# Kernel optimization log

Measured on AMD Instinct MI355X. Metric: run time of the kernel, lower is better.

## Reference

```python
import jax, jax.numpy as jnp
import numpy as np

B, N, NODE_DIM = 32, 512, 2
D, H, L, FF = 512, 8, 3, 2048
DK = D // H  # key/val dim per head = 64
EPS = 1e-5


def batch_norm(h, gamma, beta):
    # BatchNorm1d in training mode over flattened (batch*graph) dim, biased var
    flat = h.reshape(-1, h.shape[-1])
    mu = flat.mean(axis=0)
    var = flat.var(axis=0)
    out = (flat - mu) * jax.lax.rsqrt(var + EPS) * gamma + beta
    return out.reshape(h.shape)


def mha(h, Wq, Wk, Wv, Wo):
    # h: [B,N,D]; Wq/Wk/Wv: [H,D,DK]; Wo: [H,DK,D]
    Q = jnp.einsum('bnd,hdk->hbnk', h, Wq)
    K = jnp.einsum('bnd,hdk->hbnk', h, Wk)
    V = jnp.einsum('bnd,hdk->hbnk', h, Wv)
    scores = jnp.einsum('hbqk,hbnk->hbqn', Q, K) / jnp.sqrt(jnp.float32(DK))
    attn = jax.nn.softmax(scores, axis=-1)
    heads = jnp.einsum('hbqn,hbnk->hbqk', attn, V)
    return jnp.einsum('hbqk,hkd->bqd', heads, Wo)


def setup_inputs() -> dict:
    key = jax.random.key(0)
    ks = jax.random.split(key, 16)
    u = lambda k, shape, fan: jax.random.uniform(k, shape, jnp.float32, -1.0, 1.0) / np.sqrt(fan)
    return {
        'x': jax.random.normal(ks[0], (B, N, NODE_DIM), jnp.float32),
        'We': u(ks[1], (D, NODE_DIM), NODE_DIM),
        'be': u(ks[2], (D,), NODE_DIM),
        'Wq': u(ks[3], (L, H, D, DK), DK),
        'Wk': u(ks[4], (L, H, D, DK), DK),
        'Wv': u(ks[5], (L, H, D, DK), DK),
        'Wo': u(ks[6], (L, H, DK, D), D),
        'g1': jnp.ones((L, D), jnp.float32),
        'b1': jnp.zeros((L, D), jnp.float32),
        'W1': u(ks[7], (L, FF, D), D),
        'bb1': u(ks[8], (L, FF), D),
        'W2': u(ks[9], (L, D, FF), FF),
        'bb2': u(ks[10], (L, D), FF),
        'g2': jnp.ones((L, D), jnp.float32),
        'b2': jnp.zeros((L, D), jnp.float32),
    }


def reference(x, We, be, Wq, Wk, Wv, Wo, g1, b1, W1, bb1, W2, bb2, g2, b2):
    # init embed: Linear(node_dim -> D)
    h = jnp.einsum('bnc,dc->bnd', x, We) + be
    for i in range(L):
        h = batch_norm(h + mha(h, Wq[i], Wk[i], Wv[i], Wo[i]), g1[i], b1[i])
        ff = jax.nn.relu(jnp.einsum('bnd,fd->bnf', h, W1[i]) + bb1[i])
        ff = jnp.einsum('bnf,df->bnd', ff, W2[i]) + bb2[i]
        h = batch_norm(h + ff, g2[i], b2[i])
    return h, h.mean(axis=1)
```

## Files before the change

kernel.cpp:

```cpp
#include <hip/hip_runtime.h>
#include <hip/hip_bf16.h>

#define Bx 32
#define Nx 512
#define Dx 512
#define Hx 8
#define DKx 64
#define FFx 2048
#define TOK (Bx * Nx)
#define EPSx 1e-5f

typedef float  f32x4  __attribute__((ext_vector_type(4)));
typedef _Float16 hfrag8 __attribute__((ext_vector_type(8)));
typedef _Float16 h4     __attribute__((ext_vector_type(4)));

struct hf2 { _Float16 hi, lo; };
__device__ __forceinline__ hf2 split2h(float v) {
    _Float16 h = (_Float16)v;
    hf2 r; r.hi = h; r.lo = (_Float16)(v - (float)h);
    return r;
}

__device__ __forceinline__ void gl16(const void* g, void* l) {
    __builtin_amdgcn_global_load_lds(
        (const __attribute__((address_space(1))) unsigned int*)g,
        (__attribute__((address_space(3))) unsigned int*)l, 16, 0, 0);
}

__device__ __forceinline__ int swzoff(int row, int q) {
    int p = row >> 1;
    int sl = ((row & 1) << 2) | q;
    int s = sl ^ (p & 7);
    return p * 128 + s * 16;
}

__device__ __forceinline__ float ldsel(const void* p32, const void* p16, size_t i, int f32) {
    return f32 ? ((const float*)p32)[i]
               : __bfloat162float(((const __hip_bfloat16*)p16)[i]);
}

__global__ void detect_kernel(const void* __restrict__ x, int* __restrict__ flag)
{
    if (threadIdx.x == 0 && blockIdx.x == 0) {
        const unsigned short* u = (const unsigned short*)x;
        int hits = 0;
        for (int i = 0; i < 256; ++i) {
            int e = (u[i] >> 7) & 0xFF;
            if (e >= 0x86) ++hits;
        }
        *flag = (hits > 8) ? 1 : 0;
    }
}

__global__ __launch_bounds__(256) void cvt_kernel(
    const void* __restrict__ W, _Float16* __restrict__ o, const int* __restrict__ dtp)
{
    const int f32 = *dtp;
    size_t idx = (size_t)blockIdx.x * 256 + threadIdx.x;
    o[idx] = (_Float16)ldsel(W, W, idx, f32);
}

__global__ __launch_bounds__(256) void transpose_cvt_kernel(
    const void* __restrict__ W, _Float16* __restrict__ o,
    int R, int C, const int* __restrict__ dtp)
{
    const int f32 = *dtp;
    __shared__ float tile[64][65];
    const size_t mbase = (size_t)blockIdx.z * R * C;
    const int c0 = blockIdx.x * 64, r0 = blockIdx.y * 64;
    const int tc = threadIdx.x & 63, tg = threadIdx.x >> 6;
    #pragma unroll
    for (int i = 0; i < 16; ++i) {
        int r = tg * 16 + i;
        tile[r][tc] = ldsel(W, W, mbase + (size_t)(r0 + r) * C + c0 + tc, f32);
    }
    __syncthreads();
    #pragma unroll
    for (int i = 0; i < 16; ++i) {
        int cc = tg * 16 + i;
        o[mbase + (size_t)(c0 + cc) * R + r0 + tc] = (_Float16)tile[tc][cc];
    }
}

__global__ __launch_bounds__(256) void embed_kernel(
    const void* __restrict__ x, const void* __restrict__ We,
    const void* __restrict__ be, _Float16* __restrict__ hh, _Float16* __restrict__ hl,
    const int* __restrict__ dtp)
{
    const int f32 = *dtp;
    size_t idx = (size_t)blockIdx.x * 256 + threadIdx.x;
    int d = idx & (Dx - 1);
    size_t t = idx >> 9;
    float v = ldsel(x, x, t * 2, f32)     * ldsel(We, We, d * 2, f32) +
              ldsel(x, x, t * 2 + 1, f32) * ldsel(We, We, d * 2 + 1, f32) +
              ldsel(be, be, d, f32);
    hf2 s = split2h(v);
    hh[idx] = s.hi; hl[idx] = s.lo;
}

template <int NMF, int EPI, int OHF, int STATS>
__global__ __launch_bounds__(256, NMF == 2 ? 3 : 4) void gemm3(
    const _Float16* __restrict__ Ahg, const _Float16* __restrict__ Alg,
    const _Float16* __restrict__ Bg,
    const void* __restrict__ bias32, const void* __restrict__ bias16,
    const _Float16* __restrict__ residH, const _Float16* __restrict__ residL,
    void* __restrict__ outp, float* __restrict__ part,
    int M, int N, int K, const int* __restrict__ dtp)
{
    constexpr int PLANES = NMF + 1;
    constexpr int BUFB = PLANES * 8192;
    constexpr int BOFF = NMF * 8192;
    const int f32 = *dtp;
    __shared__ __align__(16) unsigned char lds[2][BUFB];

    const int tid = threadIdx.x;
    const int gx = gridDim.x;
    const int nwg = gx * gridDim.y;
    int flat = blockIdx.y * gx + blockIdx.x;
    flat = (flat & 7) * (nwg >> 3) + (flat >> 3);
    const int bm = (flat / gx) * 128;
    const int bn = (flat % gx) * 128;

    const int lane = tid & 63, wv = tid >> 6;
    const int quad = lane >> 4, lrow = lane & 15;
    const int wm = (wv & 1) * 64, wn = (wv >> 1) * 64;

    f32x4 acc[4][4] = {};

    const int s2 = (lane & 7) ^ (lane >> 3);
    const int rl = 2 * (lane >> 3) + (s2 >> 2);
    const int cl = (s2 & 3) * 8;

    const _Float16* wsrc;
    int wrb;
    bool doStage;
    if constexpr (NMF == 2) {
        doStage = (wv < 3);
        wsrc = (wv == 0) ? Ahg : (wv == 1) ? Alg : Bg;
        wrb  = (wv < 2) ? bm : bn;
    } else {
        doStage = (wv < 2);
        wsrc = (wv == 0) ? Ahg : Bg;
        wrb  = (wv == 0) ? bm : bn;
    }

    auto stage = [&](int buf, int k0) {
        if (doStage) {
            const _Float16* s = wsrc + (size_t)(wrb + rl) * K + k0 + cl;
            #pragma unroll
            for (int ch = 0; ch < 8; ++ch)
                gl16(s + (size_t)(ch * 16) * K, &lds[buf][wv * 8192 + ch * 1024]);
        }
    };

    int offA[4], offB[4];
    #pragma unroll
    for (int mt = 0; mt < 4; ++mt) offA[mt] = swzoff(wm + mt * 16 + lrow, quad);
    #pragma unroll
    for (int nt = 0; nt < 4; ++nt) offB[nt] = BOFF + swzoff(wn + nt * 16 + lrow, quad);

    stage(0, 0);
    if (32 < K) stage(1, 32);

    int cur = 0;
    for (int k0 = 0; k0 < K; k0 += 32) {
        if (k0 + 32 < K) asm volatile("s_waitcnt vmcnt(8)" ::: "memory");
        else             asm volatile("s_waitcnt vmcnt(0)" ::: "memory");
        __builtin_amdgcn_sched_barrier(0);
        __builtin_amdgcn_s_barrier();
        __builtin_amdgcn_sched_barrier(0);

        __builtin_amdgcn_s_setprio(1);
        const unsigned char* bp = lds[cur];
        hfrag8 ah[4], alo[4];
        #pragma unroll
        for (int mt = 0; mt < 4; ++mt) {
            ah[mt] = *(const hfrag8*)(bp + offA[mt]);
            if constexpr (NMF == 2) alo[mt] = *(const hfrag8*)(bp + offA[mt] + 8192);
        }
        #pragma unroll
        for (int nt = 0; nt < 4; ++nt) {
            hfrag8 b = *(const hfrag8*)(bp + offB[nt]);
            #pragma unroll
            for (int mt = 0; mt < 4; ++mt) {
                acc[mt][nt] = __builtin_amdgcn_mfma_f32_16x16x32_f16(ah[mt], b, acc[mt][nt], 0, 0, 0);
                if constexpr (NMF == 2)
                    acc[mt][nt] = __builtin_amdgcn_mfma_f32_16x16x32_f16(alo[mt], b, acc[mt][nt], 0, 0, 0);
            }
        }
        __builtin_amdgcn_s_setprio(0);

        __builtin_amdgcn_sched_barrier(0);
        asm volatile("s_waitcnt lgkmcnt(0)" ::: "memory");
        __builtin_amdgcn_s_barrier();
        __builtin_amdgcn_sched_barrier(0);

        if (k0 + 64 < K) stage(cur, k0 + 64);
        cur ^= 1;
    }

    #pragma unroll
    for (int nt = 0; nt < 4; ++nt) {
        const int n = bn + wn + nt * 16 + lrow;
        float cs = 0.f, cq = 0.f;
        #pragma unroll
        for (int mt = 0; mt < 4; ++mt)
            #pragma unroll
            for (int reg = 0; reg < 4; ++reg) {
                int m = bm + wm + mt * 16 + quad * 4 + reg;
                float v = acc[mt][nt][reg];
                if constexpr (EPI == 1) { v += ldsel(bias32, bias16, n, f32); v = fmaxf(v, 0.f); }
                if constexpr (EPI == 2) {
                    if (bias32) v += ldsel(bias32, bias16, n, f32);
                    size_t ridx = (size_t)m * N + n;
                    v += (float)residH[ridx] + (float)residL[ridx];
                }
                if constexpr (OHF) ((_Float16*)outp)[(size_t)m * N + n] = (_Float16)v;
                else               ((float*)outp)[(size_t)m * N + n] = v;
                if constexpr (STATS) { cs += v; cq += v * v; }
            }
        if constexpr (STATS) {
            cs += __shfl_xor(cs, 16); cs += __shfl_xor(cs, 32);
            cq += __shfl_xor(cq, 16); cq += __shfl_xor(cq, 32);
            if (quad == 0) {
                float* pb = part + (size_t)(bm >> 7) * 1024;
                atomicAdd(&pb[n], cs);
                atomicAdd(&pb[512 + n], cq);
            }
        }
    }
}

__global__ __launch_bounds__(256, 3) void qkv_mfma(
    const _Float16* __restrict__ Ahg, const _Float16* __restrict__ Alg,
    const _Float16* __restrict__ QT, const _Float16* __restrict__ KT,
    const _Float16* __restrict__ VT,
    _Float16* __restrict__ Qhg, _Float16* __restrict__ Qlg,
    _Float16* __restrict__ Khg, _Float16* __restrict__ Vo, int M, int K)
{
    __shared__ __align__(16) unsigned char lds[2][3 * 8192];

    const int tid = threadIdx.x;
    const int gx = gridDim.x;
    const int nwg = gx * gridDim.y;
    int flat = blockIdx.y * gx + blockIdx.x;
    flat = (flat & 7) * (nwg >> 3) + (flat >> 3);
    const int bm = (flat / gx) * 128;
    const int bn = (flat % gx) * 128;

    const int sel = bn >> 9;
    const int nloc = bn & 511;
    const _Float16* Bg = ((sel == 0) ? QT : (sel == 1) ? KT : VT) + (size_t)nloc * K;

    const int lane = tid & 63, wv = tid >> 6;
    const int quad = lane >> 4, lrow = lane & 15;
    const int wm = (wv & 1) * 64, wn = (wv >> 1) * 64;

    f32x4 acc[4][4] = {};

    const int s2 = (lane & 7) ^ (lane >> 3);
    const int rl = 2 * (lane >> 3) + (s2 >> 2);
    const int cl = (s2 & 3) * 8;

    const bool doStage = (wv < 3);
    const _Float16* wsrc = (wv == 0) ? Ahg : (wv == 1) ? Alg : Bg;
    const int wrb = (wv < 2) ? bm : 0;

    auto stage = [&](int buf, int k0) {
        if (doStage) {
            const _Float16* s = wsrc + (size_t)(wrb + rl) * K + k0 + cl;
            #pragma unroll
            for (int ch = 0; ch < 8; ++ch)
                gl16(s + (size_t)(ch * 16) * K, &lds[buf][wv * 8192 + ch * 1024]);
        }
    };

    int offA[4], offB[4];
    #pragma unroll
    for (int mt = 0; mt < 4; ++mt) offA[mt] = swzoff(wm + mt * 16 + lrow, quad);
    #pragma unroll
    for (int nt = 0; nt < 4; ++nt) offB[nt] = 16384 + swzoff(wn + nt * 16 + lrow, quad);

    stage(0, 0);
    if (32 < K) stage(1, 32);

    int cur = 0;
    for (int k0 = 0; k0 < K; k0 += 32) {
        if (k0 + 32 < K) asm volatile("s_waitcnt vmcnt(8)" ::: "memory");
        else             asm volatile("s_waitcnt vmcnt(0)" ::: "memory");
        __builtin_amdgcn_sched_barrier(0);
        __builtin_amdgcn_s_barrier();
        __builtin_amdgcn_sched_barrier(0);

        __builtin_amdgcn_s_setprio(1);
        const unsigned char* bp = lds[cur];
        hfrag8 ah[4], alo[4];
        #pragma unroll
        for (int mt = 0; mt < 4; ++mt) {
            ah[mt]  = *(const hfrag8*)(bp + offA[mt]);
            alo[mt] = *(const hfrag8*)(bp + offA[mt] + 8192);
        }
        #pragma unroll
        for (int nt = 0; nt < 4; ++nt) {
            hfrag8 b = *(const hfrag8*)(bp + offB[nt]);
            #pragma unroll
            for (int mt = 0; mt < 4; ++mt) {
                acc[mt][nt] = __builtin_amdgcn_mfma_f32_16x16x32_f16(ah[mt],  b, acc[mt][nt], 0, 0, 0);
                acc[mt][nt] = __builtin_amdgcn_mfma_f32_16x16x32_f16(alo[mt], b, acc[mt][nt], 0, 0, 0);
            }
        }
        __builtin_amdgcn_s_setprio(0);

        __builtin_amdgcn_sched_barrier(0);
        asm volatile("s_waitcnt lgkmcnt(0)" ::: "memory");
        __builtin_amdgcn_s_barrier();
        __builtin_amdgcn_sched_barrier(0);

        if (k0 + 64 < K) stage(cur, k0 + 64);
        cur ^= 1;
    }

    const int nb = M >> 9;
    #pragma unroll
    for (int mt = 0; mt < 4; ++mt)
        #pragma unroll
        for (int nt = 0; nt < 4; ++nt) {
            const int ncol = nloc + wn + nt * 16 + lrow;
            const int head = ncol >> 6, dk = ncol & 63;
            const int m0 = bm + wm + mt * 16 + quad * 4;
            const int b_ = m0 >> 9, q = m0 & 511;
            if (sel == 2) {
                h4 v;
                #pragma unroll
                for (int reg = 0; reg < 4; ++reg) v[reg] = (_Float16)acc[mt][nt][reg];
                *(h4*)&Vo[(((size_t)head * nb + b_) * DKx + dk) * Nx + q] = v;
            } else if (sel == 1) {
                #pragma unroll
                for (int reg = 0; reg < 4; ++reg) {
                    size_t oidx = (((size_t)head * nb + b_) * Nx + (q + reg)) * DKx + dk;
                    Khg[oidx] = (_Float16)acc[mt][nt][reg];
                }
            } else {
                #pragma unroll
                for (int reg = 0; reg < 4; ++reg) {
                    hf2 s = split2h(acc[mt][nt][reg]);
                    size_t oidx = (((size_t)head * nb + b_) * Nx + (q + reg)) * DKx + dk;
                    Qhg[oidx] = s.hi;
                    Qlg[oidx] = s.lo;
                }
            }
        }
}

__global__ __launch_bounds__(256, 4) void attn_kernel(
    const _Float16* __restrict__ Qhg, const _Float16* __restrict__ Qlg,
    const _Float16* __restrict__ Khg, const _Float16* __restrict__ Vtg,
    _Float16* __restrict__ headsH, _Float16* __restrict__ headsL)
{
    __shared__ __align__(16) _Float16  Kh[64][72];
    __shared__ __align__(16) _Float16  Vt[64][72];
    __shared__ __align__(16) _Float16  Sp[64][72];
    __shared__ float ml[64], ll[64], al[64];

    const int tid = threadIdx.x;
    const int q0 = blockIdx.x * 64;
    const int hb = blockIdx.y;
    const size_t base = (size_t)hb * (Nx * DKx);
    const int lane = tid & 63, wv = tid >> 6;
    const int quad = lane >> 4, lrow = lane & 15;
    const int wm = (wv & 1) * 32, wn = (wv >> 1) * 32;
    const int sr = tid >> 2, sc = (tid & 3) * 16;

    {
        size_t off = base + (size_t)(q0 + sr) * DKx + sc;
        *(hfrag8*)&Kh[sr][sc]     = *(const hfrag8*)(Qhg + off);
        *(hfrag8*)&Kh[sr][sc + 8] = *(const hfrag8*)(Qhg + off + 8);
        *(hfrag8*)&Sp[sr][sc]     = *(const hfrag8*)(Qlg + off);
        *(hfrag8*)&Sp[sr][sc + 8] = *(const hfrag8*)(Qlg + off + 8);
    }
    if (tid < 64) { ml[tid] = -INFINITY; ll[tid] = 0.f; }
    __syncthreads();

    hfrag8 qh[2][2], qlo[2][2];
    #pragma unroll
    for (int mt = 0; mt < 2; ++mt)
        #pragma unroll
        for (int ks = 0; ks < 2; ++ks) {
            qh[mt][ks]  = *(const hfrag8*)&Kh[wm + mt * 16 + lrow][ks * 32 + quad * 8];
            qlo[mt][ks] = *(const hfrag8*)&Sp[wm + mt * 16 + lrow][ks * 32 + quad * 8];
        }
    __syncthreads();

    hfrag8 pkh[2], pv[2];
    auto loadKV = [&](int n0) {
        size_t off = base + (size_t)(n0 + sr) * DKx + sc;
        pkh[0] = *(const hfrag8*)(Khg + off);
        pkh[1] = *(const hfrag8*)(Khg + off + 8);
        const _Float16* vp = Vtg + base + (size_t)sr * Nx + n0 + sc;
        pv[0] = *(const hfrag8*)vp;
        pv[1] = *(const hfrag8*)(vp + 8);
    };
    auto storeKV = [&]() {
        *(hfrag8*)&Kh[sr][sc]     = pkh[0];
        *(hfrag8*)&Kh[sr][sc + 8] = pkh[1];
        *(hfrag8*)&Vt[sr][sc]     = pv[0];
        *(hfrag8*)&Vt[sr][sc + 8] = pv[1];
    };

    f32x4 accO[2][2] = {};

    loadKV(0); storeKV();
    __syncthreads();

    for (int n0 = 0; n0 < Nx; n0 += 64) {
        const bool more = (n0 + 64 < Nx);
        if (more) loadKV(n0 + 64);

        f32x4 accS[2][2] = {};
        __builtin_amdgcn_s_setprio(1);
        #pragma unroll
        for (int ks = 0; ks < 2; ++ks) {
            hfrag8 bh[2];
            #pragma unroll
            for (int nt = 0; nt < 2; ++nt)
                bh[nt] = *(const hfrag8*)&Kh[wn + nt * 16 + lrow][ks * 32 + quad * 8];
            #pragma unroll
            for (int mt = 0; mt < 2; ++mt)
                #pragma unroll
                for (int nt = 0; nt < 2; ++nt) {
                    accS[mt][nt] = __builtin_amdgcn_mfma_f32_16x16x32_f16(qh[mt][ks],  bh[nt], accS[mt][nt], 0, 0, 0);
                    accS[mt][nt] = __builtin_amdgcn_mfma_f32_16x16x32_f16(qlo[mt][ks], bh[nt], accS[mt][nt], 0, 0, 0);
                }
        }
        __builtin_amdgcn_s_setprio(0);
        #pragma unroll
        for (int mt = 0; mt < 2; ++mt)
            #pragma unroll
            for (int nt = 0; nt < 2; ++nt)
                #pragma unroll
                for (int reg = 0; reg < 4; ++reg)
                    Sp[wm + mt * 16 + quad * 4 + reg][wn + nt * 16 + lrow] =
                        (_Float16)(accS[mt][nt][reg] * 0.125f);
        __syncthreads();

        {
            hfrag8 s0 = *(const hfrag8*)&Sp[sr][sc];
            hfrag8 s1 = *(const hfrag8*)&Sp[sr][sc + 8];
            float rmax = -INFINITY;
            #pragma unroll
            for (int j = 0; j < 8; ++j) {
                rmax = fmaxf(rmax, (float)s0[j]);
                rmax = fmaxf(rmax, (float)s1[j]);
            }
            rmax = fmaxf(rmax, __shfl_xor(rmax, 1));
            rmax = fmaxf(rmax, __shfl_xor(rmax, 2));
            float mold = ml[sr];
            float mnew = fmaxf(mold, rmax);
            float sum = 0.f;
            hfrag8 p0, p1;
            #pragma unroll
            for (int j = 0; j < 8; ++j) {
                float pa = __expf((float)s0[j] - mnew);
                float pb = __expf((float)s1[j] - mnew);
                sum += pa + pb;
                p0[j] = (_Float16)pa;
                p1[j] = (_Float16)pb;
            }
            sum += __shfl_xor(sum, 1);
            sum += __shfl_xor(sum, 2);
            *(hfrag8*)&Sp[sr][sc]     = p0;
            *(hfrag8*)&Sp[sr][sc + 8] = p1;
            if ((tid & 3) == 0) {
                float alpha = __expf(mold - mnew);
                ml[sr] = mnew;
                ll[sr] = ll[sr] * alpha + sum;
                al[sr] = alpha;
            }
        }
        __syncthreads();

        #pragma unroll
        for (int mt = 0; mt < 2; ++mt) {
            float a0 = al[wm + mt * 16 + quad * 4 + 0];
            float a1 = al[wm + mt * 16 + quad * 4 + 1];
            float a2 = al[wm + mt * 16 + quad * 4 + 2];
            float a3 = al[wm + mt * 16 + quad * 4 + 3];
            #pragma unroll
            for (int nt = 0; nt < 2; ++nt) {
                accO[mt][nt][0] *= a0; accO[mt][nt][1] *= a1;
                accO[mt][nt][2] *= a2; accO[mt][nt][3] *= a3;
            }
        }
        __builtin_amdgcn_s_setprio(1);
        #pragma unroll
        for (int ks = 0; ks < 2; ++ks) {
            hfrag8 ap[2], bv[2];
            #pragma unroll
            for (int mt = 0; mt < 2; ++mt)
                ap[mt] = *(const hfrag8*)&Sp[wm + mt * 16 + lrow][ks * 32 + quad * 8];
            #pragma unroll
            for (int nt = 0; nt < 2; ++nt)
                bv[nt] = *(const hfrag8*)&Vt[wn + nt * 16 + lrow][ks * 32 + quad * 8];
            #pragma unroll
            for (int mt = 0; mt < 2; ++mt)
                #pragma unroll
                for (int nt = 0; nt < 2; ++nt)
                    accO[mt][nt] = __builtin_amdgcn_mfma_f32_16x16x32_f16(ap[mt], bv[nt], accO[mt][nt], 0, 0, 0);
        }
        __builtin_amdgcn_s_setprio(0);

        if (more) {
            __syncthreads();
            storeKV();
            __syncthreads();
        }
    }

    const int h_ = hb >> 5, b_ = hb & 31;
    #pragma unroll
    for (int mt = 0; mt < 2; ++mt)
        #pragma unroll
        for (int reg = 0; reg < 4; ++reg) {
            int qrow = wm + mt * 16 + quad * 4 + reg;
            float invl = 1.f / ll[qrow];
            size_t tok = (size_t)b_ * Nx + (q0 + qrow);
            #pragma unroll
            for (int nt = 0; nt < 2; ++nt) {
                int dk = wn + nt * 16 + lrow;
                hf2 s = split2h(accO[mt][nt][reg] * invl);
                size_t oidx = tok * Dx + h_ * DKx + dk;
                headsH[oidx] = s.hi;
                headsL[oidx] = s.lo;
            }
        }
}

__global__ __launch_bounds__(256) void bn_final(
    const float* __restrict__ part, float* __restrict__ stats)
{
    int c = blockIdx.x * 256 + threadIdx.x;
    float s = 0.f;
    for (int rt = 0; rt < 128; ++rt) s += part[(size_t)rt * 1024 + c];
    stats[c] = s;
}

__global__ __launch_bounds__(256) void bn_norm(
    const float* __restrict__ t, const float* __restrict__ stats,
    const void* __restrict__ g32, const void* __restrict__ g16,
    const void* __restrict__ b32, const void* __restrict__ b16,
    _Float16* __restrict__ hh, _Float16* __restrict__ hl, const int* __restrict__ dtp)
{
    const int f32 = *dtp;
    size_t idx = (size_t)blockIdx.x * 256 + threadIdx.x;
    int c = idx & (Dx - 1);
    const float invM = 1.f / (float)TOK;
    float mu = stats[c] * invM;
    float var = stats[Dx + c] * invM - mu * mu;
    float v = (t[idx] - mu) * rsqrtf(var + EPSx) * ldsel(g32, g16, c, f32) + ldsel(b32, b16, c, f32);
    hf2 s = split2h(v);
    hh[idx] = s.hi; hl[idx] = s.lo;
}

__global__ __launch_bounds__(256) void out_h_kernel(
    const _Float16* __restrict__ hh, const _Float16* __restrict__ hl, float* __restrict__ out)
{
    size_t idx = (size_t)blockIdx.x * 256 + threadIdx.x;
    out[idx] = (float)hh[idx] + (float)hl[idx];
}

__global__ __launch_bounds__(256) void out_mean_part(
    const _Float16* __restrict__ hh, const _Float16* __restrict__ hl, float* __restrict__ part)
{
    int b = blockIdx.x;
    int g = blockIdx.y;
    int d = threadIdx.x;
    float s0 = 0.f, s1 = 0.f;
    for (int n = g * 64; n < g * 64 + 64; ++n) {
        size_t idx = ((size_t)b * Nx + n) * Dx;
        s0 += (float)hh[idx + d]       + (float)hl[idx + d];
        s1 += (float)hh[idx + d + 256] + (float)hl[idx + d + 256];
    }
    part[((size_t)b * 8 + g) * Dx + d]       = s0;
    part[((size_t)b * 8 + g) * Dx + d + 256] = s1;
}

__global__ __launch_bounds__(256) void out_mean_final(
    const float* __restrict__ part, float* __restrict__ out2)
{
    size_t o = (size_t)blockIdx.x * 256 + threadIdx.x;
    int b = (int)(o >> 9), d = (int)(o & 511);
    float s = 0.f;
    #pragma unroll
    for (int g = 0; g < 8; ++g) s += part[((size_t)b * 8 + g) * Dx + d];
    out2[o] = s * (1.f / (float)Nx);
}

extern "C" void kernel_launch(void* const* d_in, const int* in_sizes, int n_in,
                              void* d_out, int out_size, void* d_ws, size_t ws_size,
                              hipStream_t stream)
{
    const void* x   = d_in[0];
    const void* We  = d_in[1];
    const void* be  = d_in[2];
    const void* Wq  = d_in[3];
    const void* Wk  = d_in[4];
    const void* Wv  = d_in[5];
    const void* Wo  = d_in[6];
    const void* g1  = d_in[7];
    const void* b1  = d_in[8];
    const void* W1  = d_in[9];
    const void* bb1 = d_in[10];
    const void* W2  = d_in[11];
    const void* bb2 = d_in[12];
    const void* g2  = d_in[13];
    const void* b2  = d_in[14];

    const size_t szHD = (size_t)TOK * Dx;
    const size_t QKN  = (size_t)Hx * Bx * Nx * DKx;
    const size_t szQT = (size_t)3 * Hx * DKx * Dx;
    const size_t szW1 = (size_t)3 * FFx * Dx;
    const size_t szWqkvL = (size_t)Hx * Dx * DKx;

    float* t     = (float*)d_ws;
    float* stats = t + szHD;
    int*   dtp   = (int*)(stats + 2 * Dx);
    _Float16* hh = (_Float16*)(stats + 2 * Dx + 64);
    _Float16* hl = hh + szHD;
    _Float16* region = hl + szHD;

    _Float16* headsH = region;
    _Float16* headsL = headsH + szHD;
    _Float16* Qhg    = headsL + szHD;
    _Float16* Qlg    = Qhg + QKN;
    _Float16* Khg    = Qlg + QKN;
    _Float16* Vtg    = Khg + QKN;
    _Float16* ffbuf = region;

    _Float16* WqT = Vtg + QKN;
    _Float16* WkT = WqT + szQT;
    _Float16* WvT = WkT + szQT;
    _Float16* WoT = WvT + szQT;
    _Float16* W1c = WoT + szQT;
    _Float16* W2c = W1c + szW1;
    float*    part = (float*)(W2c + szW1);

    auto p32 = [](const void* p, size_t e) { return (const void*)((const float*)p + e); };
    auto p16 = [](const void* p, size_t e) { return (const void*)((const __hip_bfloat16*)p + e); };

    detect_kernel<<<1, 64, 0, stream>>>(x, dtp);

    transpose_cvt_kernel<<<dim3(1, 8, 24), 256, 0, stream>>>(Wq, WqT, Dx, DKx, dtp);
    transpose_cvt_kernel<<<dim3(1, 8, 24), 256, 0, stream>>>(Wk, WkT, Dx, DKx, dtp);
    transpose_cvt_kernel<<<dim3(1, 8, 24), 256, 0, stream>>>(Wv, WvT, Dx, DKx, dtp);
    transpose_cvt_kernel<<<dim3(8, 8, 3), 256, 0, stream>>>(Wo, WoT, Dx, Dx, dtp);
    cvt_kernel<<<szW1 / 256, 256, 0, stream>>>(W1, W1c, dtp);
    cvt_kernel<<<szW1 / 256, 256, 0, stream>>>(W2, W2c, dtp);

    embed_kernel<<<TOK * Dx / 256, 256, 0, stream>>>(x, We, be, hh, hl, dtp);

    const dim3 gQKV(12, TOK / 128);
    const dim3 gWo(Dx / 128, TOK / 128);
    const dim3 gAttn(Nx / 64, Hx * Bx);
    const dim3 gFF1(FFx / 128, TOK / 128);
    const dim3 gFF2(Dx / 128, TOK / 128);
    const size_t partBytes = 128 * 1024 * sizeof(float);
    for (int l = 0; l < 3; ++l) {
        const size_t eQ = (size_t)l * szWqkvL;
        const size_t e1 = (size_t)l * FFx * Dx;
        const size_t eD = (size_t)l * Dx, eF = (size_t)l * FFx;

        qkv_mfma<<<gQKV, 256, 0, stream>>>(
            hh, hl, WqT + eQ, WkT + eQ, WvT + eQ,
            Qhg, Qlg, Khg, Vtg, TOK, Dx);
        attn_kernel<<<gAttn, 256, 0, stream>>>(Qhg, Qlg, Khg, Vtg, headsH, headsL);

        hipMemsetAsync(part, 0, partBytes, stream);
        gemm3<2, 2, 0, 1><<<gWo, 256, 0, stream>>>(
            headsH, headsL, WoT + eQ,
            nullptr, nullptr, hh, hl, t, part, TOK, Dx, Dx, dtp);
        bn_final<<<4, 256, 0, stream>>>(part, stats);
        bn_norm<<<TOK * Dx / 256, 256, 0, stream>>>(
            t, stats, p32(g1, eD), p16(g1, eD), p32(b1, eD), p16(b1, eD), hh, hl, dtp);

        gemm3<2, 1, 1, 0><<<gFF1, 256, 0, stream>>>(
            hh, hl, W1c + e1,
            p32(bb1, eF), p16(bb1, eF), nullptr, nullptr, ffbuf, nullptr, TOK, FFx, Dx, dtp);
        hipMemsetAsync(part, 0, partBytes, stream);
        gemm3<1, 2, 0, 1><<<gFF2, 256, 0, stream>>>(
            ffbuf, nullptr, W2c + e1,
            p32(bb2, eD), p16(bb2, eD), hh, hl, t, part, TOK, Dx, FFx, dtp);
        bn_final<<<4, 256, 0, stream>>>(part, stats);
        bn_norm<<<TOK * Dx / 256, 256, 0, stream>>>(
            t, stats, p32(g2, eD), p16(g2, eD), p32(b2, eD), p16(b2, eD), hh, hl, dtp);
    }

    out_h_kernel<<<TOK * Dx / 256, 256, 0, stream>>>(hh, hl, (float*)d_out);
    out_mean_part<<<dim3(Bx, 8), 256, 0, stream>>>(hh, hl, part);
    out_mean_final<<<Bx * Dx / 256, 256, 0, stream>>>(part, (float*)d_out + (size_t)TOK * Dx);
}
```

Measured before the change: 1.381 ms.

## Drop low-precision split planes in QKV and Wo GEMMs, store residual as fp16 pair

The QKV GEMM now reads only the high fp16 half of the activations, and attention writes a single fp16 heads tensor, so the Wo GEMM runs single-plane with half the MFMA work. The pre-norm buffer t goes from fp32 to a hi/lo fp16 pair written by the GEMM epilogue, and the final layer's bn_norm writes the fp32 output directly, which removes the separate out_h kernel. The setprio hints are also dropped, and qkv gets a higher occupancy bound from its smaller LDS footprint. Accuracy drops in QKV inputs and heads, which could push results past tolerance.

After: 1.432 ms. 1.04x slower.

```diff
diff --git a/kernel.cpp b/kernel.cpp
--- a/kernel.cpp
+++ b/kernel.cpp
@@ -104,7 +104,7 @@
     const _Float16* __restrict__ Bg,
     const void* __restrict__ bias32, const void* __restrict__ bias16,
     const _Float16* __restrict__ residH, const _Float16* __restrict__ residL,
-    void* __restrict__ outp, float* __restrict__ part,
+    void* __restrict__ outp, void* __restrict__ outp2, float* __restrict__ part,
     int M, int N, int K, const int* __restrict__ dtp)
 {
     constexpr int PLANES = NMF + 1;
@@ -170,7 +170,6 @@
         __builtin_amdgcn_s_barrier();
         __builtin_amdgcn_sched_barrier(0);
 
-        __builtin_amdgcn_s_setprio(1);
         const unsigned char* bp = lds[cur];
         hfrag8 ah[4], alo[4];
         #pragma unroll
@@ -188,7 +187,6 @@
                     acc[mt][nt] = __builtin_amdgcn_mfma_f32_16x16x32_f16(alo[mt], b, acc[mt][nt], 0, 0, 0);
             }
         }
-        __builtin_amdgcn_s_setprio(0);
 
         __builtin_amdgcn_sched_barrier(0);
         asm volatile("s_waitcnt lgkmcnt(0)" ::: "memory");
@@ -215,8 +213,14 @@
                     size_t ridx = (size_t)m * N + n;
                     v += (float)residH[ridx] + (float)residL[ridx];
                 }
-                if constexpr (OHF) ((_Float16*)outp)[(size_t)m * N + n] = (_Float16)v;
-                else               ((float*)outp)[(size_t)m * N + n] = v;
+                size_t oidx = (size_t)m * N + n;
+                if constexpr (OHF == 1) ((_Float16*)outp)[oidx] = (_Float16)v;
+                else if constexpr (OHF == 2) {
+                    hf2 s = split2h(v);
+                    ((_Float16*)outp)[oidx]  = s.hi;
+                    ((_Float16*)outp2)[oidx] = s.lo;
+                }
+                else ((float*)outp)[oidx] = v;
                 if constexpr (STATS) { cs += v; cq += v * v; }
             }
         if constexpr (STATS) {
@@ -231,14 +235,14 @@
     }
 }
 
-__global__ __launch_bounds__(256, 3) void qkv_mfma(
-    const _Float16* __restrict__ Ahg, const _Float16* __restrict__ Alg,
+__global__ __launch_bounds__(256, 4) void qkv_mfma(
+    const _Float16* __restrict__ Ahg,
     const _Float16* __restrict__ QT, const _Float16* __restrict__ KT,
     const _Float16* __restrict__ VT,
     _Float16* __restrict__ Qhg, _Float16* __restrict__ Qlg,
     _Float16* __restrict__ Khg, _Float16* __restrict__ Vo, int M, int K)
 {
-    __shared__ __align__(16) unsigned char lds[2][3 * 8192];
+    __shared__ __align__(16) unsigned char lds[2][2 * 8192];
 
     const int tid = threadIdx.x;
     const int gx = gridDim.x;
@@ -262,9 +266,9 @@
     const int rl = 2 * (lane >> 3) + (s2 >> 2);
     const int cl = (s2 & 3) * 8;
 
-    const bool doStage = (wv < 3);
-    const _Float16* wsrc = (wv == 0) ? Ahg : (wv == 1) ? Alg : Bg;
-    const int wrb = (wv < 2) ? bm : 0;
+    const bool doStage = (wv < 2);
+    const _Float16* wsrc = (wv == 0) ? Ahg : Bg;
+    const int wrb = (wv == 0) ? bm : 0;
 
     auto stage = [&](int buf, int k0) {
         if (doStage) {
@@ -279,7 +283,7 @@
     #pragma unroll
     for (int mt = 0; mt < 4; ++mt) offA[mt] = swzoff(wm + mt * 16 + lrow, quad);
     #pragma unroll
-    for (int nt = 0; nt < 4; ++nt) offB[nt] = 16384 + swzoff(wn + nt * 16 + lrow, quad);
+    for (int nt = 0; nt < 4; ++nt) offB[nt] = 8192 + swzoff(wn + nt * 16 + lrow, quad);
 
     stage(0, 0);
     if (32 < K) stage(1, 32);
@@ -292,24 +296,18 @@
         __builtin_amdgcn_s_barrier();
         __builtin_amdgcn_sched_barrier(0);
 
-        __builtin_amdgcn_s_setprio(1);
         const unsigned char* bp = lds[cur];
-        hfrag8 ah[4], alo[4];
-        #pragma unroll
-        for (int mt = 0; mt < 4; ++mt) {
-            ah[mt]  = *(const hfrag8*)(bp + offA[mt]);
-            alo[mt] = *(const hfrag8*)(bp + offA[mt] + 8192);
-        }
+        hfrag8 ah[4];
+        #pragma unroll
+        for (int mt = 0; mt < 4; ++mt)
+            ah[mt] = *(const hfrag8*)(bp + offA[mt]);
         #pragma unroll
         for (int nt = 0; nt < 4; ++nt) {
             hfrag8 b = *(const hfrag8*)(bp + offB[nt]);
             #pragma unroll
-            for (int mt = 0; mt < 4; ++mt) {
-                acc[mt][nt] = __builtin_amdgcn_mfma_f32_16x16x32_f16(ah[mt],  b, acc[mt][nt], 0, 0, 0);
-                acc[mt][nt] = __builtin_amdgcn_mfma_f32_16x16x32_f16(alo[mt], b, acc[mt][nt], 0, 0, 0);
-            }
-        }
-        __builtin_amdgcn_s_setprio(0);
+            for (int mt = 0; mt < 4; ++mt)
+                acc[mt][nt] = __builtin_amdgcn_mfma_f32_16x16x32_f16(ah[mt], b, acc[mt][nt], 0, 0, 0);
+        }
 
         __builtin_amdgcn_sched_barrier(0);
         asm volatile("s_waitcnt lgkmcnt(0)" ::: "memory");
@@ -355,7 +353,7 @@
 __global__ __launch_bounds__(256, 4) void attn_kernel(
     const _Float16* __restrict__ Qhg, const _Float16* __restrict__ Qlg,
     const _Float16* __restrict__ Khg, const _Float16* __restrict__ Vtg,
-    _Float16* __restrict__ headsH, _Float16* __restrict__ headsL)
+    _Float16* __restrict__ heads)
 {
     __shared__ __align__(16) _Float16  Kh[64][72];
     __shared__ __align__(16) _Float16  Vt[64][72];
@@ -527,10 +525,7 @@
             #pragma unroll
             for (int nt = 0; nt < 2; ++nt) {
                 int dk = wn + nt * 16 + lrow;
-                hf2 s = split2h(accO[mt][nt][reg] * invl);
-                size_t oidx = tok * Dx + h_ * DKx + dk;
-                headsH[oidx] = s.hi;
-                headsL[oidx] = s.lo;
+                heads[tok * Dx + h_ * DKx + dk] = (_Float16)(accO[mt][nt][reg] * invl);
             }
         }
 }
@@ -545,10 +540,12 @@
 }
 
 __global__ __launch_bounds__(256) void bn_norm(
-    const float* __restrict__ t, const float* __restrict__ stats,
+    const _Float16* __restrict__ th, const _Float16* __restrict__ tl,
+    const float* __restrict__ stats,
     const void* __restrict__ g32, const void* __restrict__ g16,
     const void* __restrict__ b32, const void* __restrict__ b16,
-    _Float16* __restrict__ hh, _Float16* __restrict__ hl, const int* __restrict__ dtp)
+    _Float16* __restrict__ hh, _Float16* __restrict__ hl,
+    float* __restrict__ out32, const int* __restrict__ dtp)
 {
     const int f32 = *dtp;
     size_t idx = (size_t)blockIdx.x * 256 + threadIdx.x;
@@ -556,16 +553,11 @@
     const float invM = 1.f / (float)TOK;
     float mu = stats[c] * invM;
     float var = stats[Dx + c] * invM - mu * mu;
-    float v = (t[idx] - mu) * rsqrtf(var + EPSx) * ldsel(g32, g16, c, f32) + ldsel(b32, b16, c, f32);
+    float t = (float)th[idx] + (float)tl[idx];
+    float v = (t - mu) * rsqrtf(var + EPSx) * ldsel(g32, g16, c, f32) + ldsel(b32, b16, c, f32);
     hf2 s = split2h(v);
     hh[idx] = s.hi; hl[idx] = s.lo;
-}
-
-__global__ __launch_bounds__(256) void out_h_kernel(
-    const _Float16* __restrict__ hh, const _Float16* __restrict__ hl, float* __restrict__ out)
-{
-    size_t idx = (size_t)blockIdx.x * 256 + threadIdx.x;
-    out[idx] = (float)hh[idx] + (float)hl[idx];
+    if (out32) out32[idx] = v;
 }
 
 __global__ __launch_bounds__(256) void out_mean_part(
@@ -621,19 +613,19 @@
     const size_t szW1 = (size_t)3 * FFx * Dx;
     const size_t szWqkvL = (size_t)Hx * Dx * DKx;
 
-    float* t     = (float*)d_ws;
-    float* stats = t + szHD;
-    int*   dtp   = (int*)(stats + 2 * Dx);
-    _Float16* hh = (_Float16*)(stats + 2 * Dx + 64);
-    _Float16* hl = hh + szHD;
+    _Float16* th   = (_Float16*)d_ws;
+    _Float16* tl   = th + szHD;
+    float* stats   = (float*)(tl + szHD);
+    int*   dtp     = (int*)(stats + 2 * Dx);
+    _Float16* hh   = (_Float16*)(stats + 2 * Dx + 64);
+    _Float16* hl   = hh + szHD;
     _Float16* region = hl + szHD;
 
-    _Float16* headsH = region;
-    _Float16* headsL = headsH + szHD;
-    _Float16* Qhg    = headsL + szHD;
-    _Float16* Qlg    = Qhg + QKN;
-    _Float16* Khg    = Qlg + QKN;
-    _Float16* Vtg    = Khg + QKN;
+    _Float16* heads = region;
+    _Float16* Qhg   = heads + szHD;
+    _Float16* Qlg   = Qhg + QKN;
+    _Float16* Khg   = Qlg + QKN;
+    _Float16* Vtg   = Khg + QKN;
     _Float16* ffbuf = region;
 
     _Float16* WqT = Vtg + QKN;
@@ -668,33 +660,36 @@
         const size_t eQ = (size_t)l * szWqkvL;
         const size_t e1 = (size_t)l * FFx * Dx;
         const size_t eD = (size_t)l * Dx, eF = (size_t)l * FFx;
+        const bool last = (l == 2);
 
         qkv_mfma<<<gQKV, 256, 0, stream>>>(
-            hh, hl, WqT + eQ, WkT + eQ, WvT + eQ,
+            hh, WqT + eQ, WkT + eQ, WvT + eQ,
             Qhg, Qlg, Khg, Vtg, TOK, Dx);
-        attn_kernel<<<gAttn, 256, 0, stream>>>(Qhg, Qlg, Khg, Vtg, headsH, headsL);
+        attn_kernel<<<gAttn, 256, 0, stream>>>(Qhg, Qlg, Khg, Vtg, heads);
 
         hipMemsetAsync(part, 0, partBytes, stream);
-        gemm3<2, 2, 0, 1><<<gWo, 256, 0, stream>>>(
-            headsH, headsL, WoT + eQ,
-            nullptr, nullptr, hh, hl, t, part, TOK, Dx, Dx, dtp);
+        gemm3<1, 2, 2, 1><<<gWo, 256, 0, stream>>>(
+            heads, nullptr, WoT + eQ,
+            nullptr, nullptr, hh, hl, th, tl, part, TOK, Dx, Dx, dtp);
         bn_final<<<4, 256, 0, stream>>>(part, stats);
         bn_norm<<<TOK * Dx / 256, 256, 0, stream>>>(
-            t, stats, p32(g1, eD), p16(g1, eD), p32(b1, eD), p16(b1, eD), hh, hl, dtp);
+            th, tl, stats, p32(g1, eD), p16(g1, eD), p32(b1, eD), p16(b1, eD),
+            hh, hl, nullptr, dtp);
 
         gemm3<2, 1, 1, 0><<<gFF1, 256, 0, stream>>>(
             hh, hl, W1c + e1,
-            p32(bb1, eF), p16(bb1, eF), nullptr, nullptr, ffbuf, nullptr, TOK, FFx, Dx, dtp);
+            p32(bb1, eF), p16(bb1, eF), nullptr, nullptr, ffbuf, nullptr, nullptr,
+            TOK, FFx, Dx, dtp);
         hipMemsetAsync(part, 0, partBytes, stream);
-        gemm3<1, 2, 0, 1><<<gFF2, 256, 0, stream>>>(
+        gemm3<1, 2, 2, 1><<<gFF2, 256, 0, stream>>>(
             ffbuf, nullptr, W2c + e1,
-            p32(bb2, eD), p16(bb2, eD), hh, hl, t, part, TOK, Dx, FFx, dtp);
+            p32(bb2, eD), p16(bb2, eD), hh, hl, th, tl, part, TOK, Dx, FFx, dtp);
         bn_final<<<4, 256, 0, stream>>>(part, stats);
         bn_norm<<<TOK * Dx / 256, 256, 0, stream>>>(
-            t, stats, p32(g2, eD), p16(g2, eD), p32(b2, eD), p16(b2, eD), hh, hl, dtp);
-    }
-
-    out_h_kernel<<<TOK * Dx / 256, 256, 0, stream>>>(hh, hl, (float*)d_out);
+            th, tl, stats, p32(g2, eD), p16(g2, eD), p32(b2, eD), p16(b2, eD),
+            hh, hl, last ? (float*)d_out : nullptr, dtp);
+    }
+
     out_mean_part<<<dim3(Bx, 8), 256, 0, stream>>>(hh, hl, part);
     out_mean_final<<<Bx * Dx / 256, 256, 0, stream>>>(part, (float*)d_out + (size_t)TOK * Dx);
 }
```
